# Kernel tuning notes

Hardware: AMD Instinct MI355X
Metric: run time of the kernel (lower is better)

Reference implementation:

```python
import jax, jax.numpy as jnp
import numpy as np

N = 50000
NFEAT = 128
NHID = 64
EPS = 1e-5
NEG_SLOPE = 0.2


def gat_conv(x, src, dst, W, a_src, a_dst, b):
    # x: [N, in], W: [out, in], a_src/a_dst: [out], b: [out]
    h = x @ W.T                                   # [N, out]
    alpha_s = h @ a_src                           # [N]
    alpha_d = h @ a_dst                           # [N]
    e = jax.nn.leaky_relu(alpha_s[src] + alpha_d[dst], NEG_SLOPE)  # [E]
    # segment softmax over destination nodes
    m = jax.ops.segment_max(e, dst, num_segments=N)
    e = jnp.exp(e - m[dst])
    s = jax.ops.segment_sum(e, dst, num_segments=N)
    alpha = e / (s[dst] + 1e-16)
    out = jax.ops.segment_sum(alpha[:, None] * h[src], dst, num_segments=N)
    return out + b


def batch_norm(x, gamma, beta):
    mu = jnp.mean(x, axis=0)
    var = jnp.mean((x - mu) ** 2, axis=0)
    return gamma * (x - mu) * jax.lax.rsqrt(var + EPS) + beta


def setup_inputs() -> dict:
    key = jax.random.key(0)
    ks = jax.random.split(key, 24)
    E = 800000
    x = jax.random.normal(ks[0], (N, NFEAT), dtype=jnp.float32)
    edge_index = jax.random.randint(ks[1], (2, E), 0, N, dtype=jnp.int64)

    def lin(k, o, i):
        return jax.random.normal(k, (o, i), dtype=jnp.float32) / np.sqrt(i)

    def att(k, o):
        return jax.random.normal(k, (o,), dtype=jnp.float32) / np.sqrt(o)

    return dict(
        x=x, edge_index=edge_index,
        W1=lin(ks[2], NHID, NFEAT), a1s=att(ks[3], NHID), a1d=att(ks[4], NHID), b1=jnp.zeros((NHID,), jnp.float32),
        g1=jnp.ones((NHID,), jnp.float32), be1=jnp.zeros((NHID,), jnp.float32),
        W2=lin(ks[5], NHID, NHID), a2s=att(ks[6], NHID), a2d=att(ks[7], NHID), b2=jnp.zeros((NHID,), jnp.float32),
        g2=jnp.ones((NHID,), jnp.float32), be2=jnp.zeros((NHID,), jnp.float32),
        W3=lin(ks[8], NHID, NHID), a3s=att(ks[9], NHID), a3d=att(ks[10], NHID), b3=jnp.zeros((NHID,), jnp.float32),
        g3=jnp.ones((NHID,), jnp.float32), be3=jnp.zeros((NHID,), jnp.float32),
        W4=lin(ks[11], NFEAT, NHID), a4s=att(ks[12], NFEAT), a4d=att(ks[13], NFEAT), b4=jnp.zeros((NFEAT,), jnp.float32),
    )


def reference(x, edge_index, W1, a1s, a1d, b1, g1, be1, W2, a2s, a2d, b2, g2, be2,
              W3, a3s, a3d, b3, g3, be3, W4, a4s, a4d, b4):
    loops = jnp.arange(N, dtype=edge_index.dtype)
    src = jnp.concatenate([edge_index[0], loops])  # add self-loops (PyG default)
    dst = jnp.concatenate([edge_index[1], loops])
    # Encoder
    h = jax.nn.relu(gat_conv(x, src, dst, W1, a1s, a1d, b1))
    h = batch_norm(h, g1, be1)
    h = jax.nn.relu(gat_conv(h, src, dst, W2, a2s, a2d, b2))
    h = batch_norm(h, g2, be2)
    # Attribute decoder
    h = jax.nn.relu(gat_conv(h, src, dst, W3, a3s, a3d, b3))
    h = batch_norm(h, g3, be3)
    x_hat = jax.nn.relu(gat_conv(h, src, dst, W4, a4s, a4d, b4))
    diff = jnp.abs(x - x_hat)
    return diff, x_hat
```

## Files before the change

kernel.cpp:

```cpp
#include <hip/hip_runtime.h>
#include <math.h>

#define NND 50000
#define EPSB 1e-5f
#define SLOPE 0.2f

__device__ __forceinline__ float lrelu(float v) { return v > 0.f ? v : SLOPE * v; }

__device__ __forceinline__ ushort f2bf(float f) {
    unsigned u = __float_as_uint(f);
    unsigned r = (u + 0x7fffu + ((u >> 16) & 1u)) >> 16;
    return (ushort)r;
}

__device__ __forceinline__ void acc8(float* a, uint4 w, float e) {
    a[0] += e * __uint_as_float(w.x << 16);
    a[1] += e * __uint_as_float(w.x & 0xffff0000u);
    a[2] += e * __uint_as_float(w.y << 16);
    a[3] += e * __uint_as_float(w.y & 0xffff0000u);
    a[4] += e * __uint_as_float(w.z << 16);
    a[5] += e * __uint_as_float(w.z & 0xffff0000u);
    a[6] += e * __uint_as_float(w.w << 16);
    a[7] += e * __uint_as_float(w.w & 0xffff0000u);
}


__global__ void count_kernel(const int* __restrict__ ei, int E, int* __restrict__ cnt) {
    int e = blockIdx.x * 256 + threadIdx.x;
    if (e < E) atomicAdd(&cnt[ei[E + e]], 1);
    else if (e < E + NND) atomicAdd(&cnt[e - E], 1);
}

__global__ void scan1_kernel(const int* __restrict__ in, int n, int* __restrict__ outex,
                             int* __restrict__ bsum) {
    __shared__ int tmp[256];
    int tid = threadIdx.x;
    int i = blockIdx.x * 256 + tid;
    int v = (i < n) ? in[i] : 0;
    tmp[tid] = v;
    __syncthreads();
    for (int off = 1; off < 256; off <<= 1) {
        int t = (tid >= off) ? tmp[tid - off] : 0;
        __syncthreads();
        tmp[tid] += t;
        __syncthreads();
    }
    if (i < n) outex[i] = tmp[tid] - v;
    if (tid == 255) bsum[blockIdx.x] = tmp[255];
}

__global__ void scan2_kernel(const int* __restrict__ in, int n, int* __restrict__ outex) {
    __shared__ int tmp[256];
    int tid = threadIdx.x;
    int v = (tid < n) ? in[tid] : 0;
    tmp[tid] = v;
    __syncthreads();
    for (int off = 1; off < 256; off <<= 1) {
        int t = (tid >= off) ? tmp[tid - off] : 0;
        __syncthreads();
        tmp[tid] += t;
        __syncthreads();
    }
    if (tid < n) outex[tid] = tmp[tid] - v;
}

__global__ void scan3_kernel(int* __restrict__ rp, const int* __restrict__ boff,
                             int* __restrict__ fill, int* __restrict__ srcs, int n, int etot) {
    int i = blockIdx.x * 256 + threadIdx.x;
    if (i < n) {
        int v = rp[i] + boff[blockIdx.x];
        rp[i] = v;
        srcs[v] = i;
        fill[i] = v + 1;
    }
    if (i == 0) rp[n] = etot;
}

__global__ void scatter_edge_kernel(const int* __restrict__ ei, int E, int* __restrict__ fill,
                                    int* __restrict__ srcs) {
    int e = blockIdx.x * 256 + threadIdx.x;
    if (e < E) {
        int d = ei[E + e];
        int p = atomicAdd(&fill[d], 1);
        srcs[p] = ei[e];
    }
}


template <int K, int FOUT>
__global__ __launch_bounds__(256) void gemm_kernel(
    const float* __restrict__ X, const float* __restrict__ W, ushort* __restrict__ H, int n,
    const float* __restrict__ bnsum, const float* __restrict__ bnsq, const float* __restrict__ g,
    const float* __restrict__ be, const float* __restrict__ asrc, const float* __restrict__ adst,
    float* __restrict__ as_o, float* __restrict__ ad_o) {
    constexpr int SW = FOUT + 4;
    constexpr int SX = 68;
    constexpr int NF = FOUT / 64;
    __shared__ float Wt[64 * SW];
    __shared__ float Xt[64 * SX];
    __shared__ float bnsc[K];
    __shared__ float bnsh[K];
    const int tid = threadIdx.x;
    const int nodeBase = blockIdx.x * 64;
    const int tx = tid & 15, ty = tid >> 4;
    const bool doBN = (bnsum != nullptr);

    if (doBN) {
        const float invn = 1.f / (float)NND;
        for (int f = tid; f < K; f += 256) {
            float mu = bnsum[f] * invn;
            float var = bnsq[f] * invn - mu * mu;
            float r = rsqrtf(var + EPSB);
            float sc = g[f] * r;
            bnsc[f] = sc;
            bnsh[f] = be[f] - mu * sc;
        }
    }
    __syncthreads();

    float acc[4][4 * NF];
#pragma unroll
    for (int i = 0; i < 4; i++)
#pragma unroll
        for (int j = 0; j < 4 * NF; j++) acc[i][j] = 0.f;

    for (int kc = 0; kc < K; kc += 64) {
        for (int idx = tid; idx < FOUT * 64; idx += 256) {
            int f = idx >> 6, kk = idx & 63;
            Wt[kk * SW + f] = W[f * K + kc + kk];
        }
        for (int idx = tid; idx < 64 * 16; idx += 256) {
            int r = idx >> 4, c4 = idx & 15;
            int node = nodeBase + r;
            float4 v = make_float4(0.f, 0.f, 0.f, 0.f);
            if (node < n) {
                v = ((const float4*)X)[node * (K / 4) + (kc >> 2) + c4];
                if (doBN) {
                    int f = kc + c4 * 4;
                    v.x = v.x * bnsc[f + 0] + bnsh[f + 0];
                    v.y = v.y * bnsc[f + 1] + bnsh[f + 1];
                    v.z = v.z * bnsc[f + 2] + bnsh[f + 2];
                    v.w = v.w * bnsc[f + 3] + bnsh[f + 3];
                }
            }
            Xt[(c4 * 4 + 0) * SX + r] = v.x;
            Xt[(c4 * 4 + 1) * SX + r] = v.y;
            Xt[(c4 * 4 + 2) * SX + r] = v.z;
            Xt[(c4 * 4 + 3) * SX + r] = v.w;
        }
        __syncthreads();
#pragma unroll 16
        for (int k = 0; k < 64; k++) {
            const float4 xv = *(const float4*)(Xt + k * SX + ty * 4);
            const float4 wv = *(const float4*)(Wt + k * SW + tx * 4);
            const float xa[4] = {xv.x, xv.y, xv.z, xv.w};
            float wa[4 * NF];
            wa[0] = wv.x; wa[1] = wv.y; wa[2] = wv.z; wa[3] = wv.w;
            if constexpr (NF == 2) {
                const float4 wv2 = *(const float4*)(Wt + k * SW + 64 + tx * 4);
                wa[4] = wv2.x; wa[5] = wv2.y; wa[6] = wv2.z; wa[7] = wv2.w;
            }
#pragma unroll
            for (int i = 0; i < 4; i++)
#pragma unroll
                for (int j = 0; j < 4 * NF; j++) acc[i][j] += xa[i] * wa[j];
        }
        __syncthreads();
    }
#pragma unroll
    for (int i = 0; i < 4; i++) {
        int node = nodeBase + ty * 4 + i;
        if (node < n) {
            ushort4 o;
            o.x = f2bf(acc[i][0]); o.y = f2bf(acc[i][1]);
            o.z = f2bf(acc[i][2]); o.w = f2bf(acc[i][3]);
            ((ushort4*)H)[node * (FOUT / 4) + tx] = o;
            if constexpr (NF == 2) {
                ushort4 o2;
                o2.x = f2bf(acc[i][4]); o2.y = f2bf(acc[i][5]);
                o2.z = f2bf(acc[i][6]); o2.w = f2bf(acc[i][7]);
                ((ushort4*)H)[node * (FOUT / 4) + 16 + tx] = o2;
            }
        }
    }
    if (as_o) {
        float asv[4 * NF], adv[4 * NF];
#pragma unroll
        for (int j = 0; j < 4; j++) {
            asv[j] = asrc[tx * 4 + j];
            adv[j] = adst[tx * 4 + j];
            if constexpr (NF == 2) {
                asv[4 + j] = asrc[64 + tx * 4 + j];
                adv[4 + j] = adst[64 + tx * 4 + j];
            }
        }
#pragma unroll
        for (int i = 0; i < 4; i++) {
            int node = nodeBase + ty * 4 + i;
            float ps = 0.f, pd = 0.f;
#pragma unroll
            for (int j = 0; j < 4 * NF; j++) {
                ps += acc[i][j] * asv[j];
                pd += acc[i][j] * adv[j];
            }
#pragma unroll
            for (int off = 1; off < 16; off <<= 1) {
                ps += __shfl_xor(ps, off, 64);
                pd += __shfl_xor(pd, off, 64);
            }
            if (tx == 0 && node < n) {
                as_o[node] = ps;
                ad_o[node] = pd;
            }
        }
    }
}


template <int F, bool FINAL>
__global__ __launch_bounds__(256) void edge_kernel(
    const int* __restrict__ rp, const int* __restrict__ srcs, const float* __restrict__ as_,
    const float* __restrict__ ad_, const ushort* __restrict__ h, const float* __restrict__ bias,
    float* __restrict__ y, float* __restrict__ bnsum, float* __restrict__ bnsq,
    const float* __restrict__ xin, float* __restrict__ odiff, float* __restrict__ oxhat) {
    constexpr int GS = F / 8;
    constexpr int GPW = 64 / GS;
    const int tid = threadIdx.x;
    const int lane = tid & 63;
    const int wslot = tid >> 6;
    const int sub = lane & (GS - 1);
    const int grp = (blockIdx.x * 4 + wslot) * GPW + lane / GS;
    const int ngrp = gridDim.x * 4 * GPW;
    const float4 bA = ((const float4*)bias)[sub * 2];
    const float4 bB = ((const float4*)bias)[sub * 2 + 1];
    float st[8], qt[8];
#pragma unroll
    for (int j = 0; j < 8; j++) st[j] = qt[j] = 0.f;

    for (int row = grp; row < NND; row += ngrp) {
        const int beg = rp[row], end = rp[row + 1];
        const float ad = ad_[row];
        float a[8];
#pragma unroll
        for (int j = 0; j < 8; j++) a[j] = 0.f;
        float sw = 0.f;
        int i = beg;
        for (; i + 4 <= end; i += 4) {
            int s0 = srcs[i], s1 = srcs[i + 1], s2 = srcs[i + 2], s3 = srcs[i + 3];
            uint4 h0 = *(const uint4*)(h + (size_t)s0 * F + sub * 8);
            uint4 h1 = *(const uint4*)(h + (size_t)s1 * F + sub * 8);
            uint4 h2 = *(const uint4*)(h + (size_t)s2 * F + sub * 8);
            uint4 h3 = *(const uint4*)(h + (size_t)s3 * F + sub * 8);
            float e0 = __expf(fminf(lrelu(as_[s0] + ad), 80.f));
            float e1 = __expf(fminf(lrelu(as_[s1] + ad), 80.f));
            float e2 = __expf(fminf(lrelu(as_[s2] + ad), 80.f));
            float e3 = __expf(fminf(lrelu(as_[s3] + ad), 80.f));
            acc8(a, h0, e0);
            acc8(a, h1, e1);
            acc8(a, h2, e2);
            acc8(a, h3, e3);
            sw += (e0 + e1) + (e2 + e3);
        }
        for (; i < end; i++) {
            int s0 = srcs[i];
            uint4 h0 = *(const uint4*)(h + (size_t)s0 * F + sub * 8);
            float e0 = __expf(fminf(lrelu(as_[s0] + ad), 80.f));
            acc8(a, h0, e0);
            sw += e0;
        }
        const float inv = 1.f / (sw + 1e-16f);
        float4 ya, yb;
        ya.x = fmaxf(a[0] * inv + bA.x, 0.f);
        ya.y = fmaxf(a[1] * inv + bA.y, 0.f);
        ya.z = fmaxf(a[2] * inv + bA.z, 0.f);
        ya.w = fmaxf(a[3] * inv + bA.w, 0.f);
        yb.x = fmaxf(a[4] * inv + bB.x, 0.f);
        yb.y = fmaxf(a[5] * inv + bB.y, 0.f);
        yb.z = fmaxf(a[6] * inv + bB.z, 0.f);
        yb.w = fmaxf(a[7] * inv + bB.w, 0.f);
        if constexpr (FINAL) {
            const float4* xr = (const float4*)(xin + (size_t)row * F);
            float4 xa = xr[sub * 2], xb = xr[sub * 2 + 1];
            float4* xo = (float4*)(oxhat + (size_t)row * F);
            xo[sub * 2] = ya;
            xo[sub * 2 + 1] = yb;
            float4 da, db;
            da.x = fabsf(xa.x - ya.x); da.y = fabsf(xa.y - ya.y);
            da.z = fabsf(xa.z - ya.z); da.w = fabsf(xa.w - ya.w);
            db.x = fabsf(xb.x - yb.x); db.y = fabsf(xb.y - yb.y);
            db.z = fabsf(xb.z - yb.z); db.w = fabsf(xb.w - yb.w);
            float4* dio = (float4*)(odiff + (size_t)row * F);
            dio[sub * 2] = da;
            dio[sub * 2 + 1] = db;
        } else {
            float4* yo = (float4*)(y + (size_t)row * F);
            yo[sub * 2] = ya;
            yo[sub * 2 + 1] = yb;
            st[0] += ya.x; qt[0] += ya.x * ya.x;
            st[1] += ya.y; qt[1] += ya.y * ya.y;
            st[2] += ya.z; qt[2] += ya.z * ya.z;
            st[3] += ya.w; qt[3] += ya.w * ya.w;
            st[4] += yb.x; qt[4] += yb.x * yb.x;
            st[5] += yb.y; qt[5] += yb.y * yb.y;
            st[6] += yb.z; qt[6] += yb.z * yb.z;
            st[7] += yb.w; qt[7] += yb.w * yb.w;
        }
    }
    if constexpr (!FINAL) {
        __shared__ float redS[256][8];
        __shared__ float redQ[256][8];
#pragma unroll
        for (int j = 0; j < 8; j++) {
            redS[tid][j] = st[j];
            redQ[tid][j] = qt[j];
        }
        __syncthreads();
        if (tid < F) {
            int sb = tid >> 3, j = tid & 7;
            float ts = 0.f, tq = 0.f;
            for (int k = 0; k < 256 / GS; k++) {
                int t2 = k * GS + sb;
                ts += redS[t2][j];
                tq += redQ[t2][j];
            }
            atomicAdd(&bnsum[tid], ts);
            atomicAdd(&bnsq[tid], tq);
        }
    }
}


extern "C" void kernel_launch(void* const* d_in, const int* in_sizes, int n_in, void* d_out,
                              int out_size, void* d_ws, size_t ws_size, hipStream_t stream) {
    const float* x = (const float*)d_in[0];
    const int* ei = (const int*)d_in[1];
    const int E = in_sizes[1] / 2;
    const float* W1 = (const float*)d_in[2];
    const float* a1s = (const float*)d_in[3];
    const float* a1d = (const float*)d_in[4];
    const float* b1 = (const float*)d_in[5];
    const float* g1 = (const float*)d_in[6];
    const float* be1 = (const float*)d_in[7];
    const float* W2 = (const float*)d_in[8];
    const float* a2s = (const float*)d_in[9];
    const float* a2d = (const float*)d_in[10];
    const float* b2 = (const float*)d_in[11];
    const float* g2 = (const float*)d_in[12];
    const float* be2 = (const float*)d_in[13];
    const float* W3 = (const float*)d_in[14];
    const float* a3s = (const float*)d_in[15];
    const float* a3d = (const float*)d_in[16];
    const float* b3 = (const float*)d_in[17];
    const float* g3 = (const float*)d_in[18];
    const float* be3 = (const float*)d_in[19];
    const float* W4 = (const float*)d_in[20];
    const float* a4s = (const float*)d_in[21];
    const float* a4d = (const float*)d_in[22];
    const float* b4 = (const float*)d_in[23];

    const int Etot = E + NND;

    char* w = (char*)d_ws;
    auto alloc = [&](size_t bytes) {
        void* p = (void*)w;
        w += (bytes + 255) & ~(size_t)255;
        return p;
    };
    int* cnt = (int*)alloc((size_t)NND * 4);
    float* stats = (float*)alloc(384 * 4);
    int* rp = (int*)alloc((size_t)(NND + 1) * 4);
    int* fill = (int*)alloc((size_t)NND * 4);
    int* bsum = (int*)alloc(256 * 4);
    int* bsum2 = (int*)alloc(256 * 4);
    int* srcs = (int*)alloc((size_t)Etot * 4);
    ushort* bufH = (ushort*)alloc((size_t)NND * 128 * 2);
    float* bufY = (float*)alloc((size_t)NND * 64 * 4);
    float* asb = (float*)alloc((size_t)NND * 4);
    float* adb = (float*)alloc((size_t)NND * 4);

    const int nblk = (NND + 255) / 256;
    const int cgrid = (E + NND + 255) / 256;
    const int egrid = (E + 255) / 256;
    const int ggrid = (NND + 63) / 64;
    const int xgrid = 1024;

    hipMemsetAsync(cnt, 0, (((size_t)NND * 4 + 255) & ~(size_t)255) + 384 * 4, stream);

    count_kernel<<<cgrid, 256, 0, stream>>>(ei, E, cnt);
    scan1_kernel<<<nblk, 256, 0, stream>>>(cnt, NND, rp, bsum);
    scan2_kernel<<<1, 256, 0, stream>>>(bsum, nblk, bsum2);
    scan3_kernel<<<nblk, 256, 0, stream>>>(rp, bsum2, fill, srcs, NND, Etot);
    scatter_edge_kernel<<<egrid, 256, 0, stream>>>(ei, E, fill, srcs);

    gemm_kernel<128, 64><<<ggrid, 256, 0, stream>>>(x, W1, bufH, NND, nullptr, nullptr, nullptr,
                                                    nullptr, a1s, a1d, asb, adb);
    edge_kernel<64, false><<<xgrid, 256, 0, stream>>>(rp, srcs, asb, adb, bufH, b1, bufY,
                                                      stats + 0, stats + 64, nullptr, nullptr,
                                                      nullptr);
    gemm_kernel<64, 64><<<ggrid, 256, 0, stream>>>(bufY, W2, bufH, NND, stats + 0, stats + 64,
                                                   g1, be1, a2s, a2d, asb, adb);
    edge_kernel<64, false><<<xgrid, 256, 0, stream>>>(rp, srcs, asb, adb, bufH, b2, bufY,
                                                      stats + 128, stats + 192, nullptr, nullptr,
                                                      nullptr);
    gemm_kernel<64, 64><<<ggrid, 256, 0, stream>>>(bufY, W3, bufH, NND, stats + 128, stats + 192,
                                                   g2, be2, a3s, a3d, asb, adb);
    edge_kernel<64, false><<<xgrid, 256, 0, stream>>>(rp, srcs, asb, adb, bufH, b3, bufY,
                                                      stats + 256, stats + 320, nullptr, nullptr,
                                                      nullptr);
    float* odiff = (float*)d_out;
    float* oxhat = (float*)d_out + (size_t)NND * 128;
    gemm_kernel<64, 128><<<ggrid, 256, 0, stream>>>(bufY, W4, bufH, NND, stats + 256, stats + 320,
                                                    g3, be3, a4s, a4d, asb, adb);
    edge_kernel<128, true><<<xgrid, 256, 0, stream>>>(rp, srcs, asb, adb, bufH, b4, nullptr,
                                                      nullptr, nullptr, x, odiff, oxhat);
}
```

Before: 465.9 us.

## Build CSR via two-level destination bucketing and use nontemporal memory ops

Replaces the direct per-edge atomic scatter into CSR with a two-pass bucket sort. Edges are first binned into 256 coarse destination ranges using per-block shared-memory counters and a prefix scan, then each bucket is scattered into the CSR by one block, which keeps the fill atomics and srcs writes localized. Self-loop counting moves into the scan as a +1, and the edge kernels now use nontemporal loads for srcs and nontemporal stores for outputs, with the edge grid doubled. This adds two extra kernel launches and an 8-byte-per-edge intermediate buffer.

```diff
diff --git a/kernel.cpp b/kernel.cpp
--- a/kernel.cpp
+++ b/kernel.cpp
@@ -4,6 +4,11 @@
 #define NND 50000
 #define EPSB 1e-5f
 #define SLOPE 0.2f
+#define NB 256
+#define SBLK 128
+#define BRANGE 196
+
+typedef float vfloat4 __attribute__((ext_vector_type(4)));
 
 __device__ __forceinline__ float lrelu(float v) { return v > 0.f ? v : SLOPE * v; }
 
@@ -11,6 +16,11 @@
     unsigned u = __float_as_uint(f);
     unsigned r = (u + 0x7fffu + ((u >> 16) & 1u)) >> 16;
     return (ushort)r;
+}
+
+__device__ __forceinline__ void nt_store4(float4 v, float4* p) {
+    vfloat4 t = {v.x, v.y, v.z, v.w};
+    __builtin_nontemporal_store(t, (vfloat4*)p);
 }
 
 __device__ __forceinline__ void acc8(float* a, uint4 w, float e) {
@@ -25,10 +35,67 @@
 }
 
 
-__global__ void count_kernel(const int* __restrict__ ei, int E, int* __restrict__ cnt) {
-    int e = blockIdx.x * 256 + threadIdx.x;
-    if (e < E) atomicAdd(&cnt[ei[E + e]], 1);
-    else if (e < E + NND) atomicAdd(&cnt[e - E], 1);
+__global__ __launch_bounds__(256) void countC_kernel(const int* __restrict__ ei, int E,
+                                                     int* __restrict__ cnt, int* __restrict__ C) {
+    __shared__ int lc[NB];
+    const int tid = threadIdx.x;
+    for (int i = tid; i < NB; i += 256) lc[i] = 0;
+    __syncthreads();
+    const int per = (E + SBLK - 1) / SBLK;
+    const int beg = blockIdx.x * per;
+    const int end = min(beg + per, E);
+    for (int i = beg + tid; i < end; i += 256) {
+        int d = __builtin_nontemporal_load(&ei[E + i]);
+        atomicAdd(&cnt[d], 1);
+        atomicAdd(&lc[d / BRANGE], 1);
+    }
+    __syncthreads();
+    for (int i = tid; i < NB; i += 256) C[i * SBLK + blockIdx.x] = lc[i];
+}
+
+__global__ __launch_bounds__(1024) void scanC_kernel(int* __restrict__ C) {
+    __shared__ int ps[1024];
+    const int t = threadIdx.x;
+    int v[NB * SBLK / 1024];
+    int s = 0;
+#pragma unroll
+    for (int j = 0; j < NB * SBLK / 1024; j++) {
+        v[j] = C[t * (NB * SBLK / 1024) + j];
+        s += v[j];
+    }
+    ps[t] = s;
+    __syncthreads();
+    for (int off = 1; off < 1024; off <<= 1) {
+        int x = (t >= off) ? ps[t - off] : 0;
+        __syncthreads();
+        ps[t] += x;
+        __syncthreads();
+    }
+    int ex = ps[t] - s;
+#pragma unroll
+    for (int j = 0; j < NB * SBLK / 1024; j++) {
+        int tmp = v[j];
+        C[t * (NB * SBLK / 1024) + j] = ex;
+        ex += tmp;
+    }
+}
+
+__global__ __launch_bounds__(256) void scatter_pairs_kernel(const int* __restrict__ ei, int E,
+                                                            const int* __restrict__ C,
+                                                            unsigned long long* __restrict__ pairs) {
+    __shared__ int woff[NB];
+    const int tid = threadIdx.x;
+    for (int i = tid; i < NB; i += 256) woff[i] = C[i * SBLK + blockIdx.x];
+    __syncthreads();
+    const int per = (E + SBLK - 1) / SBLK;
+    const int beg = blockIdx.x * per;
+    const int end = min(beg + per, E);
+    for (int i = beg + tid; i < end; i += 256) {
+        int s = __builtin_nontemporal_load(&ei[i]);
+        int d = __builtin_nontemporal_load(&ei[E + i]);
+        int p = atomicAdd(&woff[d / BRANGE], 1);
+        pairs[p] = ((unsigned long long)(unsigned)d << 32) | (unsigned)s;
+    }
 }
 
 __global__ void scan1_kernel(const int* __restrict__ in, int n, int* __restrict__ outex,
@@ -36,7 +103,7 @@
     __shared__ int tmp[256];
     int tid = threadIdx.x;
     int i = blockIdx.x * 256 + tid;
-    int v = (i < n) ? in[i] : 0;
+    int v = (i < n) ? in[i] + 1 : 0;
     tmp[tid] = v;
     __syncthreads();
     for (int off = 1; off < 256; off <<= 1) {
@@ -76,13 +143,19 @@
     if (i == 0) rp[n] = etot;
 }
 
-__global__ void scatter_edge_kernel(const int* __restrict__ ei, int E, int* __restrict__ fill,
-                                    int* __restrict__ srcs) {
-    int e = blockIdx.x * 256 + threadIdx.x;
-    if (e < E) {
-        int d = ei[E + e];
+__global__ __launch_bounds__(256) void bucket_csr_kernel(const unsigned long long* __restrict__ pairs,
+                                                         int E, const int* __restrict__ C,
+                                                         int* __restrict__ fill,
+                                                         int* __restrict__ srcs) {
+    const int b = blockIdx.x;
+    const int beg = C[b * SBLK];
+    const int end = (b == NB - 1) ? E : C[(b + 1) * SBLK];
+    for (int i = beg + threadIdx.x; i < end; i += 256) {
+        unsigned long long pr = __builtin_nontemporal_load(&pairs[i]);
+        int d = (int)(pr >> 32);
+        int s = (int)(pr & 0xffffffffu);
         int p = atomicAdd(&fill[d], 1);
-        srcs[p] = ei[e];
+        srcs[p] = s;
     }
 }
 
@@ -246,7 +319,10 @@
         float sw = 0.f;
         int i = beg;
         for (; i + 4 <= end; i += 4) {
-            int s0 = srcs[i], s1 = srcs[i + 1], s2 = srcs[i + 2], s3 = srcs[i + 3];
+            int s0 = __builtin_nontemporal_load(&srcs[i]);
+            int s1 = __builtin_nontemporal_load(&srcs[i + 1]);
+            int s2 = __builtin_nontemporal_load(&srcs[i + 2]);
+            int s3 = __builtin_nontemporal_load(&srcs[i + 3]);
             uint4 h0 = *(const uint4*)(h + (size_t)s0 * F + sub * 8);
             uint4 h1 = *(const uint4*)(h + (size_t)s1 * F + sub * 8);
             uint4 h2 = *(const uint4*)(h + (size_t)s2 * F + sub * 8);
@@ -262,7 +338,7 @@
             sw += (e0 + e1) + (e2 + e3);
         }
         for (; i < end; i++) {
-            int s0 = srcs[i];
+            int s0 = __builtin_nontemporal_load(&srcs[i]);
             uint4 h0 = *(const uint4*)(h + (size_t)s0 * F + sub * 8);
             float e0 = __expf(fminf(lrelu(as_[s0] + ad), 80.f));
             acc8(a, h0, e0);
@@ -282,20 +358,20 @@
             const float4* xr = (const float4*)(xin + (size_t)row * F);
             float4 xa = xr[sub * 2], xb = xr[sub * 2 + 1];
             float4* xo = (float4*)(oxhat + (size_t)row * F);
-            xo[sub * 2] = ya;
-            xo[sub * 2 + 1] = yb;
+            nt_store4(ya, &xo[sub * 2]);
+            nt_store4(yb, &xo[sub * 2 + 1]);
             float4 da, db;
             da.x = fabsf(xa.x - ya.x); da.y = fabsf(xa.y - ya.y);
             da.z = fabsf(xa.z - ya.z); da.w = fabsf(xa.w - ya.w);
             db.x = fabsf(xb.x - yb.x); db.y = fabsf(xb.y - yb.y);
             db.z = fabsf(xb.z - yb.z); db.w = fabsf(xb.w - yb.w);
             float4* dio = (float4*)(odiff + (size_t)row * F);
-            dio[sub * 2] = da;
-            dio[sub * 2 + 1] = db;
+            nt_store4(da, &dio[sub * 2]);
+            nt_store4(db, &dio[sub * 2 + 1]);
         } else {
             float4* yo = (float4*)(y + (size_t)row * F);
-            yo[sub * 2] = ya;
-            yo[sub * 2 + 1] = yb;
+            nt_store4(ya, &yo[sub * 2]);
+            nt_store4(yb, &yo[sub * 2 + 1]);
             st[0] += ya.x; qt[0] += ya.x * ya.x;
             st[1] += ya.y; qt[1] += ya.y * ya.y;
             st[2] += ya.z; qt[2] += ya.z * ya.z;
@@ -372,6 +448,8 @@
     int* fill = (int*)alloc((size_t)NND * 4);
     int* bsum = (int*)alloc(256 * 4);
     int* bsum2 = (int*)alloc(256 * 4);
+    int* C = (int*)alloc((size_t)NB * SBLK * 4);
+    unsigned long long* pairs = (unsigned long long*)alloc((size_t)E * 8);
     int* srcs = (int*)alloc((size_t)Etot * 4);
     ushort* bufH = (ushort*)alloc((size_t)NND * 128 * 2);
     float* bufY = (float*)alloc((size_t)NND * 64 * 4);
@@ -379,18 +457,19 @@
     float* adb = (float*)alloc((size_t)NND * 4);
 
     const int nblk = (NND + 255) / 256;
-    const int cgrid = (E + NND + 255) / 256;
-    const int egrid = (E + 255) / 256;
     const int ggrid = (NND + 63) / 64;
-    const int xgrid = 1024;
-
-    hipMemsetAsync(cnt, 0, (((size_t)NND * 4 + 255) & ~(size_t)255) + 384 * 4, stream);
-
-    count_kernel<<<cgrid, 256, 0, stream>>>(ei, E, cnt);
+    const int xgrid = 2048;
+
+    hipError_t _e = hipMemsetAsync(cnt, 0, (((size_t)NND * 4 + 255) & ~(size_t)255) + 384 * 4, stream);
+    (void)_e;
+
+    countC_kernel<<<SBLK, 256, 0, stream>>>(ei, E, cnt, C);
     scan1_kernel<<<nblk, 256, 0, stream>>>(cnt, NND, rp, bsum);
     scan2_kernel<<<1, 256, 0, stream>>>(bsum, nblk, bsum2);
     scan3_kernel<<<nblk, 256, 0, stream>>>(rp, bsum2, fill, srcs, NND, Etot);
-    scatter_edge_kernel<<<egrid, 256, 0, stream>>>(ei, E, fill, srcs);
+    scanC_kernel<<<1, 1024, 0, stream>>>(C);
+    scatter_pairs_kernel<<<SBLK, 256, 0, stream>>>(ei, E, C, pairs);
+    bucket_csr_kernel<<<NB, 256, 0, stream>>>(pairs, E, C, fill, srcs);
 
     gemm_kernel<128, 64><<<ggrid, 256, 0, stream>>>(x, W1, bufH, NND, nullptr, nullptr, nullptr,
                                                     nullptr, a1s, a1d, asb, adb);
```

New measurement: 547.6 us. 1.18x slower.
